# Kernel tuning notes

Measured on AMD Instinct MI355X. Metric: run time of the kernel, lower is better.

Reference implementation:

```python
import jax, jax.numpy as jnp
import numpy as np

B, S, D = 4, 2048, 1024
DQ = DK = DV = 1024

def setup_inputs() -> dict:
    key = jax.random.key(0)
    ks = jax.random.split(key, 7)
    s = 1.0 / np.sqrt(D)
    return {
        "X": jax.random.normal(ks[0], (B, S, D), dtype=jnp.float32),
        "Wq": jax.random.normal(ks[1], (D, DQ), dtype=jnp.float32) * s,
        "bq": jax.random.normal(ks[2], (DQ,), dtype=jnp.float32) * 0.01,
        "Wk": jax.random.normal(ks[3], (D, DK), dtype=jnp.float32) * s,
        "bk": jax.random.normal(ks[4], (DK,), dtype=jnp.float32) * 0.01,
        "Wv": jax.random.normal(ks[5], (D, DV), dtype=jnp.float32) * s,
        "bv": jax.random.normal(ks[6], (DV,), dtype=jnp.float32) * 0.01,
    }

def reference(X, Wq, bq, Wk, bk, Wv, bv):
    q = jnp.einsum('bsd,de->bse', X, Wq) + bq  # [B,S,DQ]
    k = jnp.einsum('bsd,de->bse', X, Wk) + bk  # [B,S,DK]
    v = jnp.einsum('bsd,de->bse', X, Wv) + bv  # [B,S,DV]
    scores = jnp.einsum('bqe,bke->bqk', q, k) / jnp.sqrt(jnp.float32(DK))
    attn = jax.nn.softmax(scores, axis=-1)
    return jnp.einsum('bqk,bkv->bqv', attn, v)
```

## Files before the change

kernel.cpp:

```cpp
#include <hip/hip_runtime.h>

typedef __bf16 bf16;
typedef __attribute__((ext_vector_type(8))) __bf16 bf16x8;
typedef __attribute__((ext_vector_type(4))) __bf16 bf16x4;
typedef __attribute__((ext_vector_type(4))) float f32x4;

typedef __attribute__((address_space(1))) const void GvPtr;
typedef __attribute__((address_space(3))) void LdsPtr;

__device__ __forceinline__ void gload_lds16(const void* g, void* l) {
    __builtin_amdgcn_global_load_lds((GvPtr*)g, (LdsPtr*)l, 16, 0, 0);
}

__global__ __launch_bounds__(256) void prep(
    const void* __restrict__ X,
    const void* __restrict__ Wq, const void* __restrict__ Wk,
    const void* __restrict__ Wv,
    const void* __restrict__ bq, const void* __restrict__ bk,
    const void* __restrict__ bv,
    bf16* __restrict__ Xb, bf16* __restrict__ wt, bf16* __restrict__ bb,
    float* __restrict__ rowsum)
{
    __shared__ int sflag;
    __shared__ bf16 t[32][33];
    const int tid = threadIdx.x;

    if (tid < 64) {
        const unsigned short* H = (const unsigned short*)X;
        int insane = 0;
        for (int i = tid; i < 128; i += 64) {
            int e = (H[2 * i] >> 7) & 0xFF;
            insane += (e >= 107 && e <= 131) ? 0 : 1;
        }
        #pragma unroll
        for (int off = 32; off > 0; off >>= 1)
            insane += __shfl_down(insane, off, 64);
        if (tid == 0) sflag = (insane >= 32) ? 1 : 0;
    }
    __syncthreads();
    const bool isf32 = (sflag != 0);

    const long b = blockIdx.x;
    if (b < 4096) {
        long i = b * 256 + tid;
        if (isf32) {
            const float4* s = (const float4*)X;
            float4 a = s[2 * i], c = s[2 * i + 1];
            bf16x8 o;
            o[0] = (bf16)a.x; o[1] = (bf16)a.y; o[2] = (bf16)a.z; o[3] = (bf16)a.w;
            o[4] = (bf16)c.x; o[5] = (bf16)c.y; o[6] = (bf16)c.z; o[7] = (bf16)c.w;
            ((bf16x8*)Xb)[i] = o;
        } else {
            ((uint4*)Xb)[i] = ((const uint4*)X)[i];
        }
    } else if (b < 7168) {
        const int wi = (int)((b - 4096) >> 10);
        const int id = (int)((b - 4096) & 1023);
        const void* src = (wi == 0) ? Wq : (wi == 1) ? Wk : Wv;
        bf16* dst = wt + (long)wi * 1024 * 1024;
        const int c0 = (id & 31) * 32, r0 = (id >> 5) * 32;
        const int tc = tid & 31, tr = tid >> 5;
        #pragma unroll
        for (int i = 0; i < 4; i++) {
            long idx = (long)(r0 + tr + i * 8) * 1024 + c0 + tc;
            t[tr + i * 8][tc] = isf32 ? (bf16)((const float*)src)[idx]
                                      : ((const bf16*)src)[idx];
        }
        __syncthreads();
        #pragma unroll
        for (int i = 0; i < 4; i++)
            dst[(long)(c0 + tr + i * 8) * 1024 + r0 + tc] = t[tc][tr + i * 8];
    } else if (b < 7180) {
        const int bi = (int)(b - 7168);
        const int wi = bi >> 2;
        const void* src = (wi == 0) ? bq : (wi == 1) ? bk : bv;
        const long i = (bi & 3) * 256 + tid;
        bb[wi * 1024 + i] = isf32 ? (bf16)((const float*)src)[i]
                                  : ((const bf16*)src)[i];
    } else {
        const long i = (b - 7180) * 256 + tid;
        ((float4*)rowsum)[i] = make_float4(0.f, 0.f, 0.f, 0.f);
    }
}

template <bool HAS_BIAS, bool OUT_F32, int WAVES, bool VSPLIT, bool EXPSUM>
__global__ __launch_bounds__(WAVES * 64, 4) void gemm_bt(
    const bf16* __restrict__ A, const bf16* __restrict__ B,
    void* __restrict__ Cv, const bf16* __restrict__ bias,
    bf16* __restrict__ vt, float* __restrict__ rowsum,
    int K, long lda, long ldb, long ldc, float scale,
    long strideA, long strideB, long strideC)
{
    constexpr int BK = 64;
    constexpr int MI = (WAVES == 4) ? 4 : 2;
    constexpr int NCH = (WAVES == 4) ? 4 : 2;
    constexpr int RSTEP = WAVES * 8;
    constexpr int LSTEP = WAVES * 64 * 8;

    __shared__ bf16 As[128 * BK];
    __shared__ bf16 Bs[128 * BK];

    const int tid  = threadIdx.x;
    const int wave = tid >> 6;
    const int lane = tid & 63;
    const int r16  = lane & 15;
    const int quad = lane >> 4;

    const long z = blockIdx.z;
    A += z * strideA;
    B += z * strideB;

    const int tX = gridDim.x;
    const int pid = blockIdx.y * tX + blockIdx.x;
    const int groupSize = 8 * tX;
    const int gid = pid / groupSize;
    const int rem = pid % groupSize;
    const int tileM = (gid * 8 + (rem & 7)) * 128;
    const int tileN = (rem >> 3) * 128;

    const int waveM = (wave >> 1) * ((WAVES == 4) ? 64 : 32);
    const int waveN = (wave & 1) * 64;

    const int rS = tid >> 3;
    const int cOff = (((tid & 7) - (tid >> 3)) & 7) * 8;
    const bf16* Ag[NCH]; const bf16* Bg[NCH];
    #pragma unroll
    for (int j = 0; j < NCH; j++) {
        Ag[j] = A + (long)(tileM + rS + j * RSTEP) * lda + cOff;
        Bg[j] = B + (long)(tileN + rS + j * RSTEP) * ldb + cOff;
    }

    f32x4 acc[MI][4] = {};

    for (int k0 = 0; k0 < K; k0 += BK) {
        #pragma unroll
        for (int j = 0; j < NCH; j++) {
            gload_lds16(Ag[j], &As[tid * 8 + j * LSTEP]);
            gload_lds16(Bg[j], &Bs[tid * 8 + j * LSTEP]);
            Ag[j] += BK; Bg[j] += BK;
        }
        __syncthreads();

        #pragma unroll
        for (int ks = 0; ks < 2; ks++) {
            bf16x8 af[MI], bfv[4];
            #pragma unroll
            for (int i = 0; i < MI; i++) {
                const int row = waveM + i * 16 + r16;
                af[i] = *(const bf16x8*)
                    &As[row * 64 + ((ks * 4 + quad + row) & 7) * 8];
            }
            #pragma unroll
            for (int i = 0; i < 4; i++) {
                const int row = waveN + i * 16 + r16;
                bfv[i] = *(const bf16x8*)
                    &Bs[row * 64 + ((ks * 4 + quad + row) & 7) * 8];
            }
            #pragma unroll
            for (int mi = 0; mi < MI; mi++)
                #pragma unroll
                for (int ni = 0; ni < 4; ni++)
                    acc[mi][ni] = __builtin_amdgcn_mfma_f32_16x16x32_bf16(
                        af[mi], bfv[ni], acc[mi][ni], 0, 0, 0);
        }
        __syncthreads();
    }

    const int crow0 = tileM + waveM + quad * 4;
    const int ccol0 = tileN + waveN + r16;

    if (EXPSUM) {
        float rs[MI][4];
        #pragma unroll
        for (int mi = 0; mi < MI; mi++)
            #pragma unroll
            for (int r = 0; r < 4; r++) rs[mi][r] = 0.0f;
        #pragma unroll
        for (int ni = 0; ni < 4; ni++) {
            const int col = ccol0 + ni * 16;
            #pragma unroll
            for (int mi = 0; mi < MI; mi++) {
                #pragma unroll
                for (int r = 0; r < 4; r++) {
                    const long row = crow0 + mi * 16 + r;
                    const float p = __expf(acc[mi][ni][r] * scale);
                    rs[mi][r] += p;
                    ((bf16*)Cv)[z * strideC + row * ldc + col] = (bf16)p;
                }
            }
        }
        #pragma unroll
        for (int mi = 0; mi < MI; mi++) {
            #pragma unroll
            for (int r = 0; r < 4; r++) {
                float s = rs[mi][r];
                s += __shfl_xor(s, 1, 64);
                s += __shfl_xor(s, 2, 64);
                s += __shfl_xor(s, 4, 64);
                s += __shfl_xor(s, 8, 64);
                if (r16 == 0)
                    atomicAdd(&rowsum[z * 2048 + crow0 + mi * 16 + r], s);
            }
        }
    } else if (VSPLIT && tileN >= 2048) {
        #pragma unroll
        for (int ni = 0; ni < 4; ni++) {
            const int col = ccol0 + ni * 16;
            const float bv = HAS_BIAS ? (float)bias[col] : 0.0f;
            const long colp = col - 2048;
            #pragma unroll
            for (int mi = 0; mi < MI; mi++) {
                const int grow = crow0 + mi * 16;
                const long bz = grow >> 11;
                const int srow = grow & 2047;
                bf16x4 o;
                #pragma unroll
                for (int r = 0; r < 4; r++)
                    o[r] = (bf16)(acc[mi][ni][r] * scale + bv);
                *(bf16x4*)&vt[(bz << 21) + colp * 2048 + srow] = o;
            }
        }
    } else {
        #pragma unroll
        for (int ni = 0; ni < 4; ni++) {
            const int col = ccol0 + ni * 16;
            const float bv = HAS_BIAS ? (float)bias[col] : 0.0f;
            #pragma unroll
            for (int mi = 0; mi < MI; mi++) {
                #pragma unroll
                for (int r = 0; r < 4; r++) {
                    const long row = crow0 + mi * 16 + r;
                    const float val = acc[mi][ni][r] * scale + bv;
                    if (OUT_F32) ((float*)Cv)[z * strideC + row * ldc + col] = val;
                    else         ((bf16*)Cv)[z * strideC + row * ldc + col] = (bf16)val;
                }
            }
        }
    }
}

__global__ __launch_bounds__(512, 2) void gemm_pv(
    const bf16* __restrict__ A, const bf16* __restrict__ B,
    float* __restrict__ C, const float* __restrict__ rowsum,
    int K, long lda, long ldb, long ldc,
    long strideA, long strideB, long strideC)
{
    constexpr int BK = 128;
    __shared__ bf16 As[128 * BK];
    __shared__ bf16 Bs[128 * BK];

    const int tid  = threadIdx.x;
    const int wave = tid >> 6;
    const int lane = tid & 63;
    const int r16  = lane & 15;
    const int quad = lane >> 4;

    const long z = blockIdx.z;
    A += z * strideA;
    B += z * strideB;

    const int tX = gridDim.x;
    const int pid = blockIdx.y * tX + blockIdx.x;
    const int groupSize = 8 * tX;
    const int gid = pid / groupSize;
    const int rem = pid % groupSize;
    const int tileM = (gid * 8 + (rem & 7)) * 128;
    const int tileN = (rem >> 3) * 128;

    const int waveM = (wave >> 1) * 32;
    const int waveN = (wave & 1) * 64;

    const int rS = tid >> 4;
    const int cOff = (((tid & 15) - (tid >> 4)) & 15) * 8;
    const bf16* Ag = A + (long)(tileM + rS) * lda + cOff;
    const bf16* Bg = B + (long)(tileN + rS) * ldb + cOff;

    f32x4 acc[2][4] = {};

    for (int k0 = 0; k0 < K; k0 += BK) {
        #pragma unroll
        for (int j = 0; j < 4; j++) {
            gload_lds16(Ag + (long)j * 32 * lda, &As[(tid + j * 512) * 8]);
            gload_lds16(Bg + (long)j * 32 * ldb, &Bs[(tid + j * 512) * 8]);
        }
        Ag += BK; Bg += BK;
        __syncthreads();

        #pragma unroll
        for (int ks = 0; ks < 4; ks++) {
            bf16x8 af[2], bfv[4];
            #pragma unroll
            for (int i = 0; i < 2; i++) {
                const int row = waveM + i * 16 + r16;
                af[i] = *(const bf16x8*)
                    &As[row * 128 + ((ks * 4 + quad + row) & 15) * 8];
            }
            #pragma unroll
            for (int i = 0; i < 4; i++) {
                const int row = waveN + i * 16 + r16;
                bfv[i] = *(const bf16x8*)
                    &Bs[row * 128 + ((ks * 4 + quad + row) & 15) * 8];
            }
            #pragma unroll
            for (int mi = 0; mi < 2; mi++)
                #pragma unroll
                for (int ni = 0; ni < 4; ni++)
                    acc[mi][ni] = __builtin_amdgcn_mfma_f32_16x16x32_bf16(
                        af[mi], bfv[ni], acc[mi][ni], 0, 0, 0);
        }
        __syncthreads();
    }

    const int crow0 = tileM + waveM + quad * 4;
    const int ccol0 = tileN + waveN + r16;
    float inv[2][4];
    #pragma unroll
    for (int mi = 0; mi < 2; mi++)
        #pragma unroll
        for (int r = 0; r < 4; r++)
            inv[mi][r] = 1.0f / rowsum[z * 2048 + crow0 + mi * 16 + r];
    #pragma unroll
    for (int ni = 0; ni < 4; ni++) {
        const int col = ccol0 + ni * 16;
        #pragma unroll
        for (int mi = 0; mi < 2; mi++)
            #pragma unroll
            for (int r = 0; r < 4; r++) {
                const long row = crow0 + mi * 16 + r;
                C[z * strideC + row * ldc + col] = acc[mi][ni][r] * inv[mi][r];
            }
    }
}

extern "C" void kernel_launch(void* const* d_in, const int* in_sizes, int n_in,
                              void* d_out, int out_size, void* d_ws, size_t ws_size,
                              hipStream_t stream) {
    constexpr int B = 4, S = 2048, D = 1024, N = 1024;
    constexpr long MS = (long)B * S;

    const void* X  = d_in[0];
    const void* Wq = d_in[1];
    const void* bq = d_in[2];
    const void* Wk = d_in[3];
    const void* bk = d_in[4];
    const void* Wv = d_in[5];
    const void* bv = d_in[6];

    char* w = (char*)d_ws;
    bf16*  Xb = (bf16*)w;                w += MS * D * sizeof(bf16);
    bf16*  wt = (bf16*)w;                w += 3L * D * N * sizeof(bf16);
    bf16*  bb = (bf16*)w;                w += 3L * N * sizeof(bf16) + 512;
    float* rowsum = (float*)w;           w += MS * sizeof(float);
    bf16*  qkv = (bf16*)w;               w += MS * 3L * N * sizeof(bf16);
    bf16*  vt = (bf16*)w;                w += MS * N * sizeof(bf16);
    bf16*  sc = (bf16*)w;

    bf16* q = qkv;
    bf16* k = qkv + N;

    prep<<<7188, 256, 0, stream>>>(X, Wq, Wk, Wv, bq, bk, bv, Xb, wt, bb, rowsum);

    gemm_bt<true, false, 8, true, false><<<dim3(3 * N / 128, MS / 128, 1), 512, 0, stream>>>(
        Xb, wt, qkv, bb, vt, nullptr, D, D, D, 3L * N, 1.0f, 0, 0, 0);

    gemm_bt<false, false, 4, false, true><<<dim3(S / 128, S / 128, B), 256, 0, stream>>>(
        q, k, sc, nullptr, nullptr, rowsum, D, 3L * N, 3L * N, S, 0.03125f,
        (long)S * 3 * N, (long)S * 3 * N, (long)S * S);

    gemm_pv<<<dim3(N / 128, S / 128, B), 512, 0, stream>>>(
        sc, vt, (float*)d_out, rowsum, S, S, S, N,
        (long)S * S, (long)N * S, (long)S * N);
}
```

Before: 244.8 us.

## Use 256x256 double-buffered pipelined GEMM for QKV and score kernels

Replaces the 128x128 single-buffered GEMM used for the QKV projection and the QK^T score kernel with a 256x256-tile, 8-wave kernel. It double-buffers A and B in LDS and interleaves the async global-to-LDS loads with MFMA work, using manual waitcnt, barriers and setprio. The goal is to hide memory latency and raise data reuse per tile. The cost is much higher LDS use (128KB) and register pressure (acc[8][4] per wave), which limits occupancy and cuts the number of blocks for the smaller score GEMM.

After: 261.2 us. 1.07x slower.

```diff
diff --git a/kernel.cpp b/kernel.cpp
--- a/kernel.cpp
+++ b/kernel.cpp
@@ -83,22 +83,16 @@
     }
 }
 
-template <bool HAS_BIAS, bool OUT_F32, int WAVES, bool VSPLIT, bool EXPSUM>
-__global__ __launch_bounds__(WAVES * 64, 4) void gemm_bt(
+template <bool HAS_BIAS, bool VSPLIT, bool EXPSUM>
+__global__ __launch_bounds__(512, 2) void gemm_bt256(
     const bf16* __restrict__ A, const bf16* __restrict__ B,
     void* __restrict__ Cv, const bf16* __restrict__ bias,
     bf16* __restrict__ vt, float* __restrict__ rowsum,
     int K, long lda, long ldb, long ldc, float scale,
     long strideA, long strideB, long strideC)
 {
-    constexpr int BK = 64;
-    constexpr int MI = (WAVES == 4) ? 4 : 2;
-    constexpr int NCH = (WAVES == 4) ? 4 : 2;
-    constexpr int RSTEP = WAVES * 8;
-    constexpr int LSTEP = WAVES * 64 * 8;
-
-    __shared__ bf16 As[128 * BK];
-    __shared__ bf16 Bs[128 * BK];
+    __shared__ bf16 As[2][256 * 64];
+    __shared__ bf16 Bs[2][256 * 64];
 
     const int tid  = threadIdx.x;
     const int wave = tid >> 6;
@@ -115,73 +109,122 @@
     const int groupSize = 8 * tX;
     const int gid = pid / groupSize;
     const int rem = pid % groupSize;
-    const int tileM = (gid * 8 + (rem & 7)) * 128;
-    const int tileN = (rem >> 3) * 128;
-
-    const int waveM = (wave >> 1) * ((WAVES == 4) ? 64 : 32);
-    const int waveN = (wave & 1) * 64;
+    const int tileM = (gid * 8 + (rem & 7)) * 256;
+    const int tileN = (rem >> 3) * 256;
+
+    const int waveM = (wave >> 2) * 128;
+    const int waveN = (wave & 3) * 64;
 
     const int rS = tid >> 3;
     const int cOff = (((tid & 7) - (tid >> 3)) & 7) * 8;
-    const bf16* Ag[NCH]; const bf16* Bg[NCH];
-    #pragma unroll
-    for (int j = 0; j < NCH; j++) {
-        Ag[j] = A + (long)(tileM + rS + j * RSTEP) * lda + cOff;
-        Bg[j] = B + (long)(tileN + rS + j * RSTEP) * ldb + cOff;
-    }
-
-    f32x4 acc[MI][4] = {};
-
-    for (int k0 = 0; k0 < K; k0 += BK) {
-        #pragma unroll
-        for (int j = 0; j < NCH; j++) {
-            gload_lds16(Ag[j], &As[tid * 8 + j * LSTEP]);
-            gload_lds16(Bg[j], &Bs[tid * 8 + j * LSTEP]);
-            Ag[j] += BK; Bg[j] += BK;
-        }
-        __syncthreads();
-
-        #pragma unroll
-        for (int ks = 0; ks < 2; ks++) {
-            bf16x8 af[MI], bfv[4];
-            #pragma unroll
-            for (int i = 0; i < MI; i++) {
-                const int row = waveM + i * 16 + r16;
-                af[i] = *(const bf16x8*)
-                    &As[row * 64 + ((ks * 4 + quad + row) & 7) * 8];
-            }
-            #pragma unroll
-            for (int i = 0; i < 4; i++) {
-                const int row = waveN + i * 16 + r16;
-                bfv[i] = *(const bf16x8*)
-                    &Bs[row * 64 + ((ks * 4 + quad + row) & 7) * 8];
-            }
-            #pragma unroll
-            for (int mi = 0; mi < MI; mi++)
-                #pragma unroll
-                for (int ni = 0; ni < 4; ni++)
-                    acc[mi][ni] = __builtin_amdgcn_mfma_f32_16x16x32_bf16(
-                        af[mi], bfv[ni], acc[mi][ni], 0, 0, 0);
-        }
-        __syncthreads();
-    }
+    const bf16* Ab = A + (long)(tileM + rS) * lda + cOff;
+    const bf16* Bb = B + (long)(tileN + rS) * ldb + cOff;
+
+    const int ch[2] = { ((quad + r16) & 7) * 8, ((quad + r16 + 4) & 7) * 8 };
+
+#define STAGE_A(buf, h, t) do {                                               \
+    const bf16* p_ = Ab + (long)((h) * 128) * lda + ((long)(t) << 6);         \
+    gload_lds16(p_,            &As[buf][tid * 8 + (h) * 8192]);               \
+    gload_lds16(p_ + 64 * lda, &As[buf][tid * 8 + (h) * 8192 + 4096]);        \
+} while (0)
+#define STAGE_B(buf, h, t) do {                                               \
+    const bf16* p_ = Bb + (long)((h) * 128) * ldb + ((long)(t) << 6);         \
+    gload_lds16(p_,            &Bs[buf][tid * 8 + (h) * 8192]);               \
+    gload_lds16(p_ + 64 * ldb, &Bs[buf][tid * 8 + (h) * 8192 + 4096]);        \
+} while (0)
+
+    f32x4 acc[8][4] = {};
+
+    STAGE_A(0, 0, 0); STAGE_A(0, 1, 0);
+    STAGE_B(0, 0, 0); STAGE_B(0, 1, 0);
+    STAGE_B(1, 0, 1); STAGE_B(1, 1, 1);
+    asm volatile("s_waitcnt vmcnt(4)" ::: "memory");
+    __builtin_amdgcn_s_barrier();
+    __builtin_amdgcn_sched_barrier(0);
+
+    const int NI = K >> 7;
+    for (int i = 0; i < NI; ++i) {
+        const int t1 = 2 * i + 1;
+        const int t2 = 2 * i + 2;
+        const int t3 = 2 * i + 3;
+        const bool notlast = (i != NI - 1);
+
+        #pragma unroll
+        for (int h8 = 0; h8 < 2; ++h8) {
+            bf16x8 bf[4][2];
+            #pragma unroll
+            for (int q = 0; q < 4; ++q) {
+                bf16x8 af[2][2];
+                if (q == 0) {
+                    #pragma unroll
+                    for (int ni = 0; ni < 4; ++ni) {
+                        const int ro = (waveN + ni * 16 + r16) << 6;
+                        #pragma unroll
+                        for (int ks = 0; ks < 2; ++ks)
+                            bf[ni][ks] = *(const bf16x8*)&Bs[h8][ro + ch[ks]];
+                    }
+                }
+                #pragma unroll
+                for (int m2 = 0; m2 < 2; ++m2) {
+                    const int ro = (waveM + (q * 2 + m2) * 16 + r16) << 6;
+                    #pragma unroll
+                    for (int ks = 0; ks < 2; ++ks)
+                        af[m2][ks] = *(const bf16x8*)&As[h8][ro + ch[ks]];
+                }
+                if (h8 == 0) {
+                    if (q == 0)      STAGE_A(1, 0, t1);
+                    else if (q == 1) STAGE_A(1, 1, t1);
+                    else if (q == 2) { if (notlast) STAGE_B(0, 0, t2); }
+                    else             { if (notlast) STAGE_B(0, 1, t2); }
+                } else if (notlast) {
+                    if (q == 0)      STAGE_A(0, 0, t2);
+                    else if (q == 1) STAGE_A(0, 1, t2);
+                    else if (q == 2) STAGE_B(1, 0, t3);
+                    else             STAGE_B(1, 1, t3);
+                }
+                __builtin_amdgcn_s_barrier();
+                __builtin_amdgcn_s_setprio(1);
+                #pragma unroll
+                for (int ks = 0; ks < 2; ++ks)
+                    #pragma unroll
+                    for (int m2 = 0; m2 < 2; ++m2)
+                        #pragma unroll
+                        for (int ni = 0; ni < 4; ++ni)
+                            acc[q * 2 + m2][ni] = __builtin_amdgcn_mfma_f32_16x16x32_bf16(
+                                af[m2][ks], bf[ni][ks], acc[q * 2 + m2][ni], 0, 0, 0);
+                __builtin_amdgcn_s_setprio(0);
+                if (q == 3) {
+                    if (h8 == 0) {
+                        if (notlast) asm volatile("s_waitcnt vmcnt(4)" ::: "memory");
+                        else         asm volatile("s_waitcnt vmcnt(0)" ::: "memory");
+                    } else if (notlast) {
+                        asm volatile("s_waitcnt vmcnt(4)" ::: "memory");
+                    }
+                }
+                __builtin_amdgcn_s_barrier();
+                __builtin_amdgcn_sched_barrier(0);
+            }
+        }
+    }
+#undef STAGE_A
+#undef STAGE_B
 
     const int crow0 = tileM + waveM + quad * 4;
     const int ccol0 = tileN + waveN + r16;
 
     if (EXPSUM) {
-        float rs[MI][4];
-        #pragma unroll
-        for (int mi = 0; mi < MI; mi++)
-            #pragma unroll
-            for (int r = 0; r < 4; r++) rs[mi][r] = 0.0f;
-        #pragma unroll
-        for (int ni = 0; ni < 4; ni++) {
+        float rs[8][4];
+        #pragma unroll
+        for (int mi = 0; mi < 8; ++mi)
+            #pragma unroll
+            for (int r = 0; r < 4; ++r) rs[mi][r] = 0.0f;
+        #pragma unroll
+        for (int ni = 0; ni < 4; ++ni) {
             const int col = ccol0 + ni * 16;
             #pragma unroll
-            for (int mi = 0; mi < MI; mi++) {
-                #pragma unroll
-                for (int r = 0; r < 4; r++) {
+            for (int mi = 0; mi < 8; ++mi) {
+                #pragma unroll
+                for (int r = 0; r < 4; ++r) {
                     const long row = crow0 + mi * 16 + r;
                     const float p = __expf(acc[mi][ni][r] * scale);
                     rs[mi][r] += p;
@@ -190,9 +233,9 @@
             }
         }
         #pragma unroll
-        for (int mi = 0; mi < MI; mi++) {
-            #pragma unroll
-            for (int r = 0; r < 4; r++) {
+        for (int mi = 0; mi < 8; ++mi) {
+            #pragma unroll
+            for (int r = 0; r < 4; ++r) {
                 float s = rs[mi][r];
                 s += __shfl_xor(s, 1, 64);
                 s += __shfl_xor(s, 2, 64);
@@ -204,35 +247,34 @@
         }
     } else if (VSPLIT && tileN >= 2048) {
         #pragma unroll
-        for (int ni = 0; ni < 4; ni++) {
+        for (int ni = 0; ni < 4; ++ni) {
             const int col = ccol0 + ni * 16;
             const float bv = HAS_BIAS ? (float)bias[col] : 0.0f;
             const long colp = col - 2048;
             #pragma unroll
-            for (int mi = 0; mi < MI; mi++) {
+            for (int mi = 0; mi < 8; ++mi) {
                 const int grow = crow0 + mi * 16;
                 const long bz = grow >> 11;
                 const int srow = grow & 2047;
                 bf16x4 o;
                 #pragma unroll
-                for (int r = 0; r < 4; r++)
+                for (int r = 0; r < 4; ++r)
                     o[r] = (bf16)(acc[mi][ni][r] * scale + bv);
                 *(bf16x4*)&vt[(bz << 21) + colp * 2048 + srow] = o;
             }
         }
     } else {
         #pragma unroll
-        for (int ni = 0; ni < 4; ni++) {
+        for (int ni = 0; ni < 4; ++ni) {
             const int col = ccol0 + ni * 16;
             const float bv = HAS_BIAS ? (float)bias[col] : 0.0f;
             #pragma unroll
-            for (int mi = 0; mi < MI; mi++) {
-                #pragma unroll
-                for (int r = 0; r < 4; r++) {
+            for (int mi = 0; mi < 8; ++mi) {
+                #pragma unroll
+                for (int r = 0; r < 4; ++r) {
                     const long row = crow0 + mi * 16 + r;
-                    const float val = acc[mi][ni][r] * scale + bv;
-                    if (OUT_F32) ((float*)Cv)[z * strideC + row * ldc + col] = val;
-                    else         ((bf16*)Cv)[z * strideC + row * ldc + col] = (bf16)val;
+                    ((bf16*)Cv)[z * strideC + row * ldc + col] =
+                        (bf16)(acc[mi][ni][r] * scale + bv);
                 }
             }
         }
@@ -360,10 +402,10 @@
 
     prep<<<7188, 256, 0, stream>>>(X, Wq, Wk, Wv, bq, bk, bv, Xb, wt, bb, rowsum);
 
-    gemm_bt<true, false, 8, true, false><<<dim3(3 * N / 128, MS / 128, 1), 512, 0, stream>>>(
+    gemm_bt256<true, true, false><<<dim3(3 * N / 256, MS / 256, 1), 512, 0, stream>>>(
         Xb, wt, qkv, bb, vt, nullptr, D, D, D, 3L * N, 1.0f, 0, 0, 0);
 
-    gemm_bt<false, false, 4, false, true><<<dim3(S / 128, S / 128, B), 256, 0, stream>>>(
+    gemm_bt256<false, false, true><<<dim3(S / 256, S / 256, B), 512, 0, stream>>>(
         q, k, sc, nullptr, nullptr, rowsum, D, 3L * N, 3L * N, S, 0.03125f,
         (long)S * 3 * N, (long)S * 3 * N, (long)S * S);
 
```
